# Kernel optimization log

Measured on AMD Instinct MI355X. Metric: run time of the kernel, lower is better.

Reference implementation:

```python
import jax, jax.numpy as jnp
import numpy as np

N_NODES = 100000


def _mean_aggregate(feat, src, dst, num_nodes):
    # mean over edges (src -> dst) of feat[src], grouped by dst; 0 for isolated nodes
    summed = jax.ops.segment_sum(feat[src], dst, num_segments=num_nodes)  # [N, d]
    deg = jax.ops.segment_sum(jnp.ones((src.shape[0],), feat.dtype), dst,
                              num_segments=num_nodes)  # [N]
    return summed / jnp.maximum(deg, 1.0)[:, None]


def setup_inputs() -> dict:
    key = jax.random.key(0)
    k1, k2, k3 = jax.random.split(key, 3)
    feat = jax.random.normal(k1, (N_NODES, 128), dtype=jnp.float32)
    # fc_self_neigh weight: Linear(3*in_feats=384 -> out_feats=128), no bias
    W = jax.random.normal(k2, (128, 384), dtype=jnp.float32) * 0.05
    edge_index = jax.random.randint(k3, (2, 800000), 0, N_NODES, dtype=jnp.int32)
    return {"feat": feat, "W": W, "edge_index": edge_index}


def reference(feat, W, edge_index):
    src, dst = edge_index[0], edge_index[1]
    n = feat.shape[0]
    h_self = feat  # feat_drop = 0.0
    # forward SAGE: mean of in-neighbor (source) features per destination node
    fwd_neigh = _mean_aggregate(feat, src, dst, n)
    # backward SAGE on reversed graph: mean of out-neighbor (dest) features per source node
    bwd_neigh = _mean_aggregate(feat, dst, src, n)
    h = jnp.concatenate((h_self, fwd_neigh, bwd_neigh), axis=1)  # [N, 3*d]
    rst = h @ W.T  # [N, out_feats], bias=False
    return jax.nn.relu(rst)
```

## Files before the change

### kernel.cpp

```cpp
#include <hip/hip_runtime.h>
#include <hip/hip_bf16.h>

#define D 128
#define CHUNK 1024
#define NXCD 8

typedef __attribute__((ext_vector_type(8))) short bf16x8;
typedef __attribute__((ext_vector_type(4))) float f32x4;

__device__ inline float bflo(unsigned u) { return __uint_as_float(u << 16); }
__device__ inline float bfhi(unsigned u) { return __uint_as_float(u & 0xffff0000u); }
__device__ inline unsigned short f2bf(float f) {
    __hip_bfloat16 h = __float2bfloat16(f);
    return *reinterpret_cast<unsigned short*>(&h);
}
__device__ inline unsigned pack2bf(float lo, float hi) {
    return (unsigned)f2bf(lo) | ((unsigned)f2bf(hi) << 16);
}

__global__ __launch_bounds__(256) void convert_kernel(
    const float* __restrict__ feat, unsigned short* __restrict__ featb, int n4f,
    const float* __restrict__ W, unsigned short* __restrict__ Wb, int n4w)
{
    int i = blockIdx.x * blockDim.x + threadIdx.x;
    const int stride = gridDim.x * blockDim.x;
    const int n4 = n4f + n4w;
    for (; i < n4; i += stride) {
        const float* x; unsigned short* y; int j;
        if (i < n4f) { x = feat; y = featb; j = i; }
        else         { x = W;    y = Wb;    j = i - n4f; }
        float4 v = *reinterpret_cast<const float4*>(&x[(size_t)j * 4]);
        uint2 o;
        o.x = pack2bf(v.x, v.y);
        o.y = pack2bf(v.z, v.w);
        *reinterpret_cast<uint2*>(&y[(size_t)j * 4]) = o;
    }
}

__global__ __launch_bounds__(256) void hist_rank_kernel(
    const int* __restrict__ src, const int* __restrict__ dst,
    int* __restrict__ cnt, int* __restrict__ rankF, int* __restrict__ rankB,
    int E, int N)
{
    const int e = blockIdx.x * blockDim.x + threadIdx.x;
    if (e < E) {
        rankF[e] = atomicAdd(&cnt[dst[e]], 1);
        rankB[e] = atomicAdd(&cnt[N + src[e]], 1);
    }
}

__global__ __launch_bounds__(256) void scan1_kernel(
    const int* __restrict__ cnt, int* __restrict__ blk, int n2)
{
    __shared__ int red[256];
    const int b = blockIdx.x, t = threadIdx.x;
    const int base = b * CHUNK + t * 4;
    int s = 0;
    if (base + 3 < n2) {
        int4 v = *reinterpret_cast<const int4*>(&cnt[base]);
        s = v.x + v.y + v.z + v.w;
    } else {
        for (int j = 0; j < 4; ++j) { int idx = base + j; if (idx < n2) s += cnt[idx]; }
    }
    red[t] = s; __syncthreads();
    for (int o = 128; o > 0; o >>= 1) { if (t < o) red[t] += red[t + o]; __syncthreads(); }
    if (t == 0) blk[b] = red[0];
}

__global__ __launch_bounds__(256) void scan3_kernel(
    const int* __restrict__ cnt, const int* __restrict__ blk,
    int* __restrict__ off, int n2, int total, int NB)
{
    __shared__ int sh[256];
    __shared__ int bs[256];
    const int b = blockIdx.x, t = threadIdx.x;

    bs[t] = (t < NB) ? blk[t] : 0;
    __syncthreads();
    for (int o = 1; o < 256; o <<= 1) {
        int v = (t >= o) ? bs[t - o] : 0;
        __syncthreads();
        bs[t] += v;
        __syncthreads();
    }
    const int blkpref = (b > 0) ? bs[b - 1] : 0;

    const int base = b * CHUNK + t * 4;
    int v[4]; int s = 0;
    for (int j = 0; j < 4; ++j) { int idx = base + j; v[j] = (idx < n2) ? cnt[idx] : 0; s += v[j]; }
    sh[t] = s; __syncthreads();
    for (int o = 1; o < 256; o <<= 1) {
        int x = (t >= o) ? sh[t - o] : 0;
        __syncthreads();
        sh[t] += x;
        __syncthreads();
    }
    int excl = blkpref + ((t > 0) ? sh[t - 1] : 0);
    for (int j = 0; j < 4; ++j) {
        int idx = base + j;
        if (idx < n2) off[idx] = excl;
        excl += v[j];
    }
    if (b == 0 && t == 0) off[n2] = total;
}

__global__ __launch_bounds__(256) void scatter_ids_kernel(
    const int* __restrict__ src, const int* __restrict__ dst,
    const int* __restrict__ off,
    const int* __restrict__ rankF, const int* __restrict__ rankB,
    int* __restrict__ csr, int E, int N, int npr)
{
    const int grp = blockIdx.x & (NXCD - 1);
    const int bIn = blockIdx.x >> 3;
    const int nbk = gridDim.x >> 3;
    const int lo = grp * npr;
    const int hi = lo + npr;

    int i = bIn * 256 + threadIdx.x;
    const int stride = nbk * 256;
    for (int e = i; e < E; e += stride) {
        const int s = src[e];
        const int d = dst[e];
        if (d >= lo && d < hi) {
            csr[off[d] + rankF[e]] = s;
        }
        if (s >= lo && s < hi) {
            csr[off[N + s] + rankB[e]] = d;
        }
    }
}

__global__ __launch_bounds__(256) void gather_mean_kernel(
    const unsigned short* __restrict__ featb, const int* __restrict__ off,
    const int* __restrict__ csr, unsigned short* __restrict__ meanb, int n2)
{
    const int tid = blockIdx.x * 256 + threadIdx.x;
    const int seg = tid >> 4;
    const int l = tid & 15;
    if (seg >= n2) return;

    const int beg = off[seg], end = off[seg + 1];
    float a0=0,a1=0,a2=0,a3=0,a4=0,a5=0,a6=0,a7=0;

    int e = beg;
    for (; e + 3 < end; e += 4) {
        const int n0 = csr[e], n1 = csr[e + 1], n2i = csr[e + 2], n3 = csr[e + 3];
        const uint4 v0 = *reinterpret_cast<const uint4*>(featb + (size_t)n0 * D + l * 8);
        const uint4 v1 = *reinterpret_cast<const uint4*>(featb + (size_t)n1 * D + l * 8);
        const uint4 v2 = *reinterpret_cast<const uint4*>(featb + (size_t)n2i * D + l * 8);
        const uint4 v3 = *reinterpret_cast<const uint4*>(featb + (size_t)n3 * D + l * 8);
        a0 += (bflo(v0.x) + bflo(v1.x)) + (bflo(v2.x) + bflo(v3.x));
        a1 += (bfhi(v0.x) + bfhi(v1.x)) + (bfhi(v2.x) + bfhi(v3.x));
        a2 += (bflo(v0.y) + bflo(v1.y)) + (bflo(v2.y) + bflo(v3.y));
        a3 += (bfhi(v0.y) + bfhi(v1.y)) + (bfhi(v2.y) + bfhi(v3.y));
        a4 += (bflo(v0.z) + bflo(v1.z)) + (bflo(v2.z) + bflo(v3.z));
        a5 += (bfhi(v0.z) + bfhi(v1.z)) + (bfhi(v2.z) + bfhi(v3.z));
        a6 += (bflo(v0.w) + bflo(v1.w)) + (bflo(v2.w) + bflo(v3.w));
        a7 += (bfhi(v0.w) + bfhi(v1.w)) + (bfhi(v2.w) + bfhi(v3.w));
    }
    for (; e < end; ++e) {
        const int n0 = csr[e];
        const uint4 v0 = *reinterpret_cast<const uint4*>(featb + (size_t)n0 * D + l * 8);
        a0 += bflo(v0.x); a1 += bfhi(v0.x);
        a2 += bflo(v0.y); a3 += bfhi(v0.y);
        a4 += bflo(v0.z); a5 += bfhi(v0.z);
        a6 += bflo(v0.w); a7 += bfhi(v0.w);
    }

    const int deg = end - beg;
    const float inv = 1.0f / (float)((deg > 1) ? deg : 1);
    uint4 o;
    o.x = pack2bf(a0 * inv, a1 * inv);
    o.y = pack2bf(a2 * inv, a3 * inv);
    o.z = pack2bf(a4 * inv, a5 * inv);
    o.w = pack2bf(a6 * inv, a7 * inv);
    *reinterpret_cast<uint4*>(meanb + (size_t)seg * D + l * 8) = o;
}

__global__ __launch_bounds__(512) void mfma_gemm_kernel(
    const unsigned short* __restrict__ featb,
    const unsigned short* __restrict__ meanb,
    const unsigned short* __restrict__ Wb,
    float* __restrict__ out, int N)
{
    __shared__ unsigned short wlds[2][128 * 128];

    const int t = threadIdx.x;
    const int wv = t >> 6;
    const int lane = t & 63;
    const int r = lane & 15;
    const int q = lane >> 4;

    const int row0 = blockIdx.x * 128 + wv * 16;
    const int row = row0 + r;
    const int rowc = (row < N) ? row : (N - 1);

    const unsigned short* h0 = featb + (size_t)rowc * D;
    const unsigned short* h1 = meanb + (size_t)rowc * D;
    const unsigned short* h2 = meanb + ((size_t)N + rowc) * D;
    bf16x8 af[12];
#pragma unroll
    for (int kk = 0; kk < 4; ++kk) {
        af[kk]     = *reinterpret_cast<const bf16x8*>(h0 + kk * 32 + q * 8);
        af[4 + kk] = *reinterpret_cast<const bf16x8*>(h1 + kk * 32 + q * 8);
        af[8 + kk] = *reinterpret_cast<const bf16x8*>(h2 + kk * 32 + q * 8);
    }

    const int sc = t >> 2;
    const int sq = t & 3;
    const char* wsrc = reinterpret_cast<const char*>(Wb) + (size_t)sc * 768;
    const int swz = (sc & 7) << 4;

    f32x4 acc[8];
#pragma unroll
    for (int n = 0; n < 8; ++n) acc[n] = (f32x4){0.f, 0.f, 0.f, 0.f};

    {
        uint4 st[4];
#pragma unroll
        for (int j = 0; j < 4; ++j)
            st[j] = *reinterpret_cast<const uint4*>(wsrc + j * 64 + sq * 16);
        char* wb0 = reinterpret_cast<char*>(&wlds[0][0]) + sc * 256;
#pragma unroll
        for (int j = 0; j < 4; ++j)
            *reinterpret_cast<uint4*>(wb0 + ((j * 64 + sq * 16) ^ swz)) = st[j];
    }
    __syncthreads();

#pragma unroll
    for (int ci = 0; ci < 3; ++ci) {
        uint4 nx[4];
        if (ci < 2) {
#pragma unroll
            for (int j = 0; j < 4; ++j)
                nx[j] = *reinterpret_cast<const uint4*>(
                    wsrc + (ci + 1) * 256 + j * 64 + sq * 16);
        }

        const char* wl = reinterpret_cast<const char*>(&wlds[ci & 1][0]);
#pragma unroll
        for (int kk = 0; kk < 4; ++kk) {
            const bf16x8 bh = af[ci * 4 + kk];
#pragma unroll
            for (int n = 0; n < 8; ++n) {
                const int c = n * 16 + r;
                const bf16x8 aw = *reinterpret_cast<const bf16x8*>(
                    wl + c * 256 + ((kk * 64 + q * 16) ^ ((c & 7) << 4)));
                acc[n] = __builtin_amdgcn_mfma_f32_16x16x32_bf16(aw, bh, acc[n], 0, 0, 0);
            }
        }

        if (ci < 2) {
            char* wbn = reinterpret_cast<char*>(&wlds[(ci + 1) & 1][0]) + sc * 256;
#pragma unroll
            for (int j = 0; j < 4; ++j)
                *reinterpret_cast<uint4*>(wbn + ((j * 64 + sq * 16) ^ swz)) = nx[j];
            __syncthreads();
        }
    }

    if (row < N) {
        float* orow = out + (size_t)row * D;
#pragma unroll
        for (int n = 0; n < 8; ++n) {
            float4 v;
            v.x = fmaxf(acc[n][0], 0.0f);
            v.y = fmaxf(acc[n][1], 0.0f);
            v.z = fmaxf(acc[n][2], 0.0f);
            v.w = fmaxf(acc[n][3], 0.0f);
            *reinterpret_cast<float4*>(orow + n * 16 + q * 4) = v;
        }
    }
}

extern "C" void kernel_launch(void* const* d_in, const int* in_sizes, int n_in,
                              void* d_out, int out_size, void* d_ws, size_t ws_size,
                              hipStream_t stream) {
    const float* feat = (const float*)d_in[0];
    const float* W    = (const float*)d_in[1];
    const int*   ei   = (const int*)d_in[2];
    float*       out  = (float*)d_out;

    const int E = in_sizes[2] / 2;
    const int N = in_sizes[0] / D;
    const int n2 = 2 * N;
    const int* src = ei;
    const int* dst = ei + E;

    int* cnt   = (int*)d_ws;
    int* off   = cnt + n2;
    int* blk   = off + (n2 + 4);
    int* rankF = blk + 256;
    int* rankB = rankF + E;
    int* csr   = rankB + E;
    unsigned short* featb = (unsigned short*)(csr + 2 * E);
    unsigned short* Wb    = featb + (size_t)N * D;
    unsigned short* meanb = Wb + 128 * 384;

    hipMemsetAsync(cnt, 0, (size_t)n2 * sizeof(int), stream);

    const int NB = (n2 + CHUNK - 1) / CHUNK;
    const int npr = (N + NXCD - 1) / NXCD;
    const int n4f = N * D / 4;
    const int n4w = 128 * 384 / 4;

    convert_kernel<<<2048, 256, 0, stream>>>(feat, featb, n4f, W, Wb, n4w);
    hist_rank_kernel<<<(E + 255) / 256, 256, 0, stream>>>(src, dst, cnt,
                                                          rankF, rankB, E, N);

    scan1_kernel<<<NB, 256, 0, stream>>>(cnt, blk, n2);
    scan3_kernel<<<NB, 256, 0, stream>>>(cnt, blk, off, n2, 2 * E, NB);
    scatter_ids_kernel<<<2048, 256, 0, stream>>>(src, dst, off, rankF, rankB,
                                                 csr, E, N, npr);

    const int gather_blocks = (n2 * 16 + 255) / 256;
    gather_mean_kernel<<<gather_blocks, 256, 0, stream>>>(featb, off, csr, meanb, n2);

    mfma_gemm_kernel<<<(N + 127) / 128, 512, 0, stream>>>(featb, meanb, Wb, out, N);
}
```

Before: 227.2 us.

## Split bf16 features into 8 column-blocked planes for cache-local gathers

Stores the bf16 feature and mean buffers as 8 separate planes of 16 columns each. The gather kernel assigns consecutive blocks to different column planes (blockIdx & 7), so each plane of about 3.2 MB is meant to stay resident in one XCD's L2 during the random neighbour gathers. The convert and GEMM kernels are changed to write and read this blocked layout. In exchange, each gather thread handles only 16 bytes per neighbour, so the CSR indices are read 8 times, and the GEMM A-loads become strided across planes.

```diff
diff --git a/kernel.cpp b/kernel.cpp
--- a/kernel.cpp
+++ b/kernel.cpp
@@ -19,21 +19,35 @@
 }
 
 __global__ __launch_bounds__(256) void convert_kernel(
-    const float* __restrict__ feat, unsigned short* __restrict__ featb, int n4f,
+    const float* __restrict__ feat, unsigned short* __restrict__ featB, int N,
     const float* __restrict__ W, unsigned short* __restrict__ Wb, int n4w)
 {
-    int i = blockIdx.x * blockDim.x + threadIdx.x;
-    const int stride = gridDim.x * blockDim.x;
-    const int n4 = n4f + n4w;
-    for (; i < n4; i += stride) {
-        const float* x; unsigned short* y; int j;
-        if (i < n4f) { x = feat; y = featb; j = i; }
-        else         { x = W;    y = Wb;    j = i - n4f; }
-        float4 v = *reinterpret_cast<const float4*>(&x[(size_t)j * 4]);
-        uint2 o;
-        o.x = pack2bf(v.x, v.y);
-        o.y = pack2bf(v.z, v.w);
-        *reinterpret_cast<uint2*>(&y[(size_t)j * 4]) = o;
+    const int b = blockIdx.y;
+    const int i = blockIdx.x * 256 + threadIdx.x;
+    if (b < 8) {
+        if (i < N) {
+            const float* sp = feat + (size_t)i * D + b * 16;
+            float4 v0 = *reinterpret_cast<const float4*>(sp + 0);
+            float4 v1 = *reinterpret_cast<const float4*>(sp + 4);
+            float4 v2 = *reinterpret_cast<const float4*>(sp + 8);
+            float4 v3 = *reinterpret_cast<const float4*>(sp + 12);
+            uint4 o0, o1;
+            o0.x = pack2bf(v0.x, v0.y); o0.y = pack2bf(v0.z, v0.w);
+            o0.z = pack2bf(v1.x, v1.y); o0.w = pack2bf(v1.z, v1.w);
+            o1.x = pack2bf(v2.x, v2.y); o1.y = pack2bf(v2.z, v2.w);
+            o1.z = pack2bf(v3.x, v3.y); o1.w = pack2bf(v3.z, v3.w);
+            unsigned short* dp = featB + (size_t)b * N * 16 + (size_t)i * 16;
+            *reinterpret_cast<uint4*>(dp + 0) = o0;
+            *reinterpret_cast<uint4*>(dp + 8) = o1;
+        }
+    } else {
+        if (i < n4w) {
+            float4 v = *reinterpret_cast<const float4*>(W + (size_t)i * 4);
+            uint2 o;
+            o.x = pack2bf(v.x, v.y);
+            o.y = pack2bf(v.z, v.w);
+            *reinterpret_cast<uint2*>(Wb + (size_t)i * 4) = o;
+        }
     }
 }
 
@@ -131,24 +145,26 @@
 }
 
 __global__ __launch_bounds__(256) void gather_mean_kernel(
-    const unsigned short* __restrict__ featb, const int* __restrict__ off,
-    const int* __restrict__ csr, unsigned short* __restrict__ meanb, int n2)
-{
-    const int tid = blockIdx.x * 256 + threadIdx.x;
-    const int seg = tid >> 4;
-    const int l = tid & 15;
+    const unsigned short* __restrict__ featB, const int* __restrict__ off,
+    const int* __restrict__ csr, unsigned short* __restrict__ meanB,
+    int n2, int N)
+{
+    const int g = blockIdx.x & 7;
+    const int seg = (blockIdx.x >> 3) * 128 + (threadIdx.x >> 1);
+    const int half = threadIdx.x & 1;
     if (seg >= n2) return;
 
+    const unsigned short* fb = featB + (size_t)g * N * 16 + half * 8;
     const int beg = off[seg], end = off[seg + 1];
     float a0=0,a1=0,a2=0,a3=0,a4=0,a5=0,a6=0,a7=0;
 
     int e = beg;
     for (; e + 3 < end; e += 4) {
         const int n0 = csr[e], n1 = csr[e + 1], n2i = csr[e + 2], n3 = csr[e + 3];
-        const uint4 v0 = *reinterpret_cast<const uint4*>(featb + (size_t)n0 * D + l * 8);
-        const uint4 v1 = *reinterpret_cast<const uint4*>(featb + (size_t)n1 * D + l * 8);
-        const uint4 v2 = *reinterpret_cast<const uint4*>(featb + (size_t)n2i * D + l * 8);
-        const uint4 v3 = *reinterpret_cast<const uint4*>(featb + (size_t)n3 * D + l * 8);
+        const uint4 v0 = *reinterpret_cast<const uint4*>(fb + (size_t)n0 * 16);
+        const uint4 v1 = *reinterpret_cast<const uint4*>(fb + (size_t)n1 * 16);
+        const uint4 v2 = *reinterpret_cast<const uint4*>(fb + (size_t)n2i * 16);
+        const uint4 v3 = *reinterpret_cast<const uint4*>(fb + (size_t)n3 * 16);
         a0 += (bflo(v0.x) + bflo(v1.x)) + (bflo(v2.x) + bflo(v3.x));
         a1 += (bfhi(v0.x) + bfhi(v1.x)) + (bfhi(v2.x) + bfhi(v3.x));
         a2 += (bflo(v0.y) + bflo(v1.y)) + (bflo(v2.y) + bflo(v3.y));
@@ -160,7 +176,7 @@
     }
     for (; e < end; ++e) {
         const int n0 = csr[e];
-        const uint4 v0 = *reinterpret_cast<const uint4*>(featb + (size_t)n0 * D + l * 8);
+        const uint4 v0 = *reinterpret_cast<const uint4*>(fb + (size_t)n0 * 16);
         a0 += bflo(v0.x); a1 += bfhi(v0.x);
         a2 += bflo(v0.y); a3 += bfhi(v0.y);
         a4 += bflo(v0.z); a5 += bfhi(v0.z);
@@ -174,12 +190,12 @@
     o.y = pack2bf(a2 * inv, a3 * inv);
     o.z = pack2bf(a4 * inv, a5 * inv);
     o.w = pack2bf(a6 * inv, a7 * inv);
-    *reinterpret_cast<uint4*>(meanb + (size_t)seg * D + l * 8) = o;
+    *reinterpret_cast<uint4*>(meanB + (size_t)g * n2 * 16 + (size_t)seg * 16 + half * 8) = o;
 }
 
 __global__ __launch_bounds__(512) void mfma_gemm_kernel(
-    const unsigned short* __restrict__ featb,
-    const unsigned short* __restrict__ meanb,
+    const unsigned short* __restrict__ featB,
+    const unsigned short* __restrict__ meanB,
     const unsigned short* __restrict__ Wb,
     float* __restrict__ out, int N)
 {
@@ -194,16 +210,22 @@
     const int row0 = blockIdx.x * 128 + wv * 16;
     const int row = row0 + r;
     const int rowc = (row < N) ? row : (N - 1);
-
-    const unsigned short* h0 = featb + (size_t)rowc * D;
-    const unsigned short* h1 = meanb + (size_t)rowc * D;
-    const unsigned short* h2 = meanb + ((size_t)N + rowc) * D;
+    const int n2 = 2 * N;
+
+    const int b2 = q >> 1;
+    const int c8 = (q & 1) * 8;
+    const size_t FB = (size_t)N * 16;
+    const size_t MB = (size_t)n2 * 16;
+    const size_t rf = (size_t)rowc * 16 + c8;
+    const size_t rb = (size_t)(N + rowc) * 16 + c8;
+
     bf16x8 af[12];
 #pragma unroll
     for (int kk = 0; kk < 4; ++kk) {
-        af[kk]     = *reinterpret_cast<const bf16x8*>(h0 + kk * 32 + q * 8);
-        af[4 + kk] = *reinterpret_cast<const bf16x8*>(h1 + kk * 32 + q * 8);
-        af[8 + kk] = *reinterpret_cast<const bf16x8*>(h2 + kk * 32 + q * 8);
+        const int blk = kk * 2 + b2;
+        af[kk]     = *reinterpret_cast<const bf16x8*>(featB + blk * FB + rf);
+        af[4 + kk] = *reinterpret_cast<const bf16x8*>(meanB + blk * MB + rf);
+        af[8 + kk] = *reinterpret_cast<const bf16x8*>(meanB + blk * MB + rb);
     }
 
     const int sc = t >> 2;
@@ -293,18 +315,18 @@
     int* rankF = blk + 256;
     int* rankB = rankF + E;
     int* csr   = rankB + E;
-    unsigned short* featb = (unsigned short*)(csr + 2 * E);
-    unsigned short* Wb    = featb + (size_t)N * D;
-    unsigned short* meanb = Wb + 128 * 384;
+    unsigned short* featB = (unsigned short*)(csr + 2 * E);
+    unsigned short* Wb    = featB + (size_t)8 * N * 16;
+    unsigned short* meanB = Wb + 128 * 384;
 
     hipMemsetAsync(cnt, 0, (size_t)n2 * sizeof(int), stream);
 
     const int NB = (n2 + CHUNK - 1) / CHUNK;
     const int npr = (N + NXCD - 1) / NXCD;
-    const int n4f = N * D / 4;
     const int n4w = 128 * 384 / 4;
 
-    convert_kernel<<<2048, 256, 0, stream>>>(feat, featb, n4f, W, Wb, n4w);
+    dim3 cgrid((N + 255) / 256, 9);
+    convert_kernel<<<cgrid, 256, 0, stream>>>(feat, featB, N, W, Wb, n4w);
     hist_rank_kernel<<<(E + 255) / 256, 256, 0, stream>>>(src, dst, cnt,
                                                           rankF, rankB, E, N);
 
@@ -313,8 +335,9 @@
     scatter_ids_kernel<<<2048, 256, 0, stream>>>(src, dst, off, rankF, rankB,
                                                  csr, E, N, npr);
 
-    const int gather_blocks = (n2 * 16 + 255) / 256;
-    gather_mean_kernel<<<gather_blocks, 256, 0, stream>>>(featb, off, csr, meanb, n2);
-
-    mfma_gemm_kernel<<<(N + 127) / 128, 512, 0, stream>>>(featb, meanb, Wb, out, N);
-}
+    const int gather_blocks = ((n2 + 127) / 128) * 8;
+    gather_mean_kernel<<<gather_blocks, 256, 0, stream>>>(featB, off, csr,
+                                                          meanB, n2, N);
+
+    mfma_gemm_kernel<<<(N + 127) / 128, 512, 0, stream>>>(featB, meanB, Wb, out, N);
+}
```

Measured after the change: 246.3 us. 1.08x slower.
